# Performance work log

Measured on AMD Instinct MI355X. Metric: run time of the kernel, lower is better.

Reference implementation:

```python
import jax, jax.numpy as jnp
import numpy as np

B, T, P, F = 32, 12, 128, 128          # batch, timesteps, n_patches, nhid
NODES_PER_PATCH = 64
HORIZON = 12
N_NODES = P * NODES_PER_PATCH          # 8192


def setup_inputs() -> dict:
    key = jax.random.key(0)
    k1, k2, k3, k4 = jax.random.split(key, 4)
    x = jax.random.normal(k1, (B, T, P, F), dtype=jnp.float32)
    # per-patch Linear weights/biases, stacked: W[p] maps (nhid*T) -> (nodes_p*horizon)
    W = jax.random.normal(k2, (P, T * F, NODES_PER_PATCH * HORIZON), dtype=jnp.float32) * 0.02
    b = jax.random.normal(k3, (P, NODES_PER_PATCH * HORIZON), dtype=jnp.float32) * 0.02
    # patch -> global node indices; a permutation (each node in exactly one patch)
    patch_node_map = jax.random.permutation(k4, jnp.arange(N_NODES, dtype=jnp.int64)).reshape(P, NODES_PER_PATCH)
    return {"x": x, "W": W, "b": b, "patch_node_map": patch_node_map}


def reference(x, W, b, patch_node_map):
    # rearrange 'b t p f -> b p (t f)'
    xr = jnp.transpose(x, (0, 2, 1, 3)).reshape(x.shape[0], P, T * F)
    # grouped GEMM: one Linear per patch
    out = jnp.einsum('bpi,pio->bpo', xr, W) + b          # [B, P, nodes*H]
    out = out.reshape(x.shape[0], P * NODES_PER_PATCH, HORIZON)
    # scatter patch-local node predictions to global node positions
    out_all = jnp.zeros((x.shape[0], N_NODES, HORIZON), dtype=x.dtype)
    out_all = out_all.at[:, patch_node_map.reshape(-1), :].set(out)
    return out_all
```

## Files before the change

kernel.cpp:

```cpp
#include <hip/hip_runtime.h>


constexpr int BATCH  = 32;
constexpr int T      = 12;
constexpr int P      = 128;
constexpr int F      = 128;
constexpr int K      = T * F;
constexpr int N      = 768;
constexpr int NPP    = 64;
constexpr int H      = 12;
constexpr int NNODES = P * NPP;
constexpr int BN     = 128;
constexpr int BK     = 64;
constexpr int NT     = N / BN;

typedef __attribute__((ext_vector_type(8))) short  bf16x8;
typedef __attribute__((ext_vector_type(4))) float  f32x4;

__device__ inline short f2bf(float f) {
    unsigned u = __float_as_uint(f);
    u += 0x7fffu + ((u >> 16) & 1u);
    return (short)(u >> 16);
}

__global__ __launch_bounds__(256, 2)
void patch_readout_kernel(const float* __restrict__ x,
                          const float* __restrict__ W,
                          const float* __restrict__ bias,
                          const int*   __restrict__ map,
                          float*       __restrict__ out)
{
    __shared__ short As[2][32 * 64];

    const int p    = blockIdx.y;
    const int n0   = blockIdx.x * BN;
    const int tid  = threadIdx.x;
    const int lane = tid & 63;
    const int wv   = tid >> 6;
    const int r    = lane & 15;
    const int c    = lane >> 4;

    const int sm  = tid >> 3;
    const int skq = tid & 7;
    const float* xrow = x + (size_t)sm * T * P * F + (size_t)p * F;
    const int abyte = (sm * 128 + skq * 16) ^ ((sm & 7) << 4);

    const float* wbase = W + (size_t)p * K * N + (size_t)(8 * c) * N + (n0 + wv * 32 + r);

    f32x4 acc[2][2] = {};
    char* asbase = (char*)&As[0][0];

    int buf = 0;
    for (int k0 = 0; k0 < K; k0 += BK, buf ^= 1) {
        const int t  = k0 >> 7;
        const int fb = k0 & 127;
        const f32x4* xp = (const f32x4*)(xrow + (size_t)t * P * F + fb + skq * 8);
        f32x4 v0 = xp[0];
        f32x4 v1 = xp[1];
        bf16x8 av;
        av[0] = f2bf(v0.x); av[1] = f2bf(v0.y); av[2] = f2bf(v0.z); av[3] = f2bf(v0.w);
        av[4] = f2bf(v1.x); av[5] = f2bf(v1.y); av[6] = f2bf(v1.z); av[7] = f2bf(v1.w);
        *(bf16x8*)(asbase + buf * 4096 + abyte) = av;

        bf16x8 bfr[2][2];
        #pragma unroll
        for (int kc = 0; kc < 2; ++kc) {
            #pragma unroll
            for (int ni = 0; ni < 2; ++ni) {
                const float* wp = wbase + (size_t)(k0 + kc * 32) * N + ni * 16;
                #pragma unroll
                for (int j = 0; j < 8; ++j)
                    bfr[kc][ni][j] = f2bf(wp[(size_t)j * N]);
            }
        }

        __syncthreads();

        bf16x8 afr[2][2];
        #pragma unroll
        for (int mi = 0; mi < 2; ++mi) {
            #pragma unroll
            for (int kc = 0; kc < 2; ++kc) {
                int m    = mi * 16 + r;
                int byte = (m * 128 + kc * 64 + c * 16) ^ ((m & 7) << 4);
                afr[mi][kc] = *(const bf16x8*)(asbase + buf * 4096 + byte);
            }
        }

        #pragma unroll
        for (int mi = 0; mi < 2; ++mi)
            #pragma unroll
            for (int ni = 0; ni < 2; ++ni)
                #pragma unroll
                for (int kc = 0; kc < 2; ++kc)
                    acc[mi][ni] = __builtin_amdgcn_mfma_f32_16x16x32_bf16(
                        afr[mi][kc], bfr[kc][ni], acc[mi][ni], 0, 0, 0);
    }

    #pragma unroll
    for (int ni = 0; ni < 2; ++ni) {
        const int col = n0 + wv * 32 + ni * 16 + r;
        const int nl  = col / H;
        const int h   = col - nl * H;
        const int g   = map[p * NPP + nl];
        const float bv = bias[p * N + col];
        #pragma unroll
        for (int mi = 0; mi < 2; ++mi) {
            #pragma unroll
            for (int i = 0; i < 4; ++i) {
                const int b = mi * 16 + c * 4 + i;
                out[((size_t)b * NNODES + g) * H + h] = acc[mi][ni][i] + bv;
            }
        }
    }
}

extern "C" void kernel_launch(void* const* d_in, const int* in_sizes, int n_in,
                              void* d_out, int out_size, void* d_ws, size_t ws_size,
                              hipStream_t stream) {
    const float* x    = (const float*)d_in[0];
    const float* W    = (const float*)d_in[1];
    const float* bias = (const float*)d_in[2];
    const int*   map  = (const int*)d_in[3];
    float*       out  = (float*)d_out;

    dim3 grid(NT, P);
    dim3 block(256);
    patch_readout_kernel<<<grid, block, 0, stream>>>(x, W, bias, map, out);
}
```

Baseline: 130.3 us.

## Stage X in two large LDS halves and software-pipeline W register loads

The per-step double-buffered A tile is replaced by staging half of the activation K range (768) into LDS at once, with only two block-wide barriers mid-loop instead of one per K step. W loads are software-pipelined into two register buffers (wA/wB), so global loads for the next step are in flight during the current step's MFMAs. Launch bounds go from 2 to 3 waves per SIMD. The cost is a 48KB LDS footprint and 64 extra VGPRs of prefetch buffers, which may limit occupancy or cause spills.

```diff
diff --git a/kernel.cpp b/kernel.cpp
--- a/kernel.cpp
+++ b/kernel.cpp
@@ -1,7 +1,6 @@
 #include <hip/hip_runtime.h>
 
 
-constexpr int BATCH  = 32;
 constexpr int T      = 12;
 constexpr int P      = 128;
 constexpr int F      = 128;
@@ -11,8 +10,10 @@
 constexpr int H      = 12;
 constexpr int NNODES = P * NPP;
 constexpr int BN     = 128;
-constexpr int BK     = 64;
 constexpr int NT     = N / BN;
+constexpr int KH     = 768;
+constexpr int TPF    = T * P * F;
+constexpr int PF     = P * F;
 
 typedef __attribute__((ext_vector_type(8))) short  bf16x8;
 typedef __attribute__((ext_vector_type(4))) float  f32x4;
@@ -23,14 +24,15 @@
     return (short)(u >> 16);
 }
 
-__global__ __launch_bounds__(256, 2)
+__global__ __launch_bounds__(256, 3)
 void patch_readout_kernel(const float* __restrict__ x,
                           const float* __restrict__ W,
                           const float* __restrict__ bias,
                           const int*   __restrict__ map,
                           float*       __restrict__ out)
 {
-    __shared__ short As[2][32 * 64];
+    __shared__ short As[32 * KH];
+    char* lds = (char*)&As[0];
 
     const int p    = blockIdx.y;
     const int n0   = blockIdx.x * BN;
@@ -40,52 +42,41 @@
     const int r    = lane & 15;
     const int c    = lane >> 4;
 
-    const int sm  = tid >> 3;
-    const int skq = tid & 7;
-    const float* xrow = x + (size_t)sm * T * P * F + (size_t)p * F;
-    const int abyte = (sm * 128 + skq * 16) ^ ((sm & 7) << 4);
-
-    const float* wbase = W + (size_t)p * K * N + (size_t)(8 * c) * N + (n0 + wv * 32 + r);
+    const float* wb = W + (size_t)p * K * N + (size_t)(8 * c) * N + (n0 + wv * 32 + r);
 
     f32x4 acc[2][2] = {};
-    char* asbase = (char*)&As[0][0];
 
-    int buf = 0;
-    for (int k0 = 0; k0 < K; k0 += BK, buf ^= 1) {
-        const int t  = k0 >> 7;
-        const int fb = k0 & 127;
-        const f32x4* xp = (const f32x4*)(xrow + (size_t)t * P * F + fb + skq * 8);
-        f32x4 v0 = xp[0];
-        f32x4 v1 = xp[1];
-        bf16x8 av;
-        av[0] = f2bf(v0.x); av[1] = f2bf(v0.y); av[2] = f2bf(v0.z); av[3] = f2bf(v0.w);
-        av[4] = f2bf(v1.x); av[5] = f2bf(v1.y); av[6] = f2bf(v1.z); av[7] = f2bf(v1.w);
-        *(bf16x8*)(asbase + buf * 4096 + abyte) = av;
+    auto issueW = [&](int k0, float* wd) {
+        #pragma unroll
+        for (int kc = 0; kc < 2; ++kc)
+            #pragma unroll
+            for (int ni = 0; ni < 2; ++ni)
+                #pragma unroll
+                for (int j = 0; j < 8; ++j)
+                    wd[kc * 16 + ni * 8 + j] = wb[(size_t)(k0 + kc * 32 + j) * N + ni * 16];
+    };
 
+    auto computeStep = [&](int k0, const float* wd) {
         bf16x8 bfr[2][2];
         #pragma unroll
-        for (int kc = 0; kc < 2; ++kc) {
+        for (int kc = 0; kc < 2; ++kc)
             #pragma unroll
-            for (int ni = 0; ni < 2; ++ni) {
-                const float* wp = wbase + (size_t)(k0 + kc * 32) * N + ni * 16;
+            for (int ni = 0; ni < 2; ++ni)
                 #pragma unroll
                 for (int j = 0; j < 8; ++j)
-                    bfr[kc][ni][j] = f2bf(wp[(size_t)j * N]);
-            }
-        }
+                    bfr[kc][ni][j] = f2bf(wd[kc * 16 + ni * 8 + j]);
 
-        __syncthreads();
-
+        const int kl = (k0 >= KH) ? (k0 - KH) : k0;
+        const int kb = kl * 2;
         bf16x8 afr[2][2];
         #pragma unroll
-        for (int mi = 0; mi < 2; ++mi) {
+        for (int mi = 0; mi < 2; ++mi)
             #pragma unroll
             for (int kc = 0; kc < 2; ++kc) {
-                int m    = mi * 16 + r;
-                int byte = (m * 128 + kc * 64 + c * 16) ^ ((m & 7) << 4);
-                afr[mi][kc] = *(const bf16x8*)(asbase + buf * 4096 + byte);
+                int row  = mi * 16 + r;
+                int byte = row * (KH * 2) + ((kb + kc * 64 + c * 16) ^ ((row & 7) << 4));
+                afr[mi][kc] = *(const bf16x8*)(lds + byte);
             }
-        }
 
         #pragma unroll
         for (int mi = 0; mi < 2; ++mi)
@@ -95,6 +86,45 @@
                 for (int kc = 0; kc < 2; ++kc)
                     acc[mi][ni] = __builtin_amdgcn_mfma_f32_16x16x32_bf16(
                         afr[mi][kc], bfr[kc][ni], acc[mi][ni], 0, 0, 0);
+    };
+
+    auto stageX = [&](int half) {
+        const int row = tid >> 3;
+        const int sub = tid & 7;
+        const float* xr = x + (size_t)row * TPF + (size_t)p * F;
+        #pragma unroll
+        for (int ci = 0; ci < 12; ++ci) {
+            int k  = ci * 64 + sub * 8;
+            int kg = half * KH + k;
+            int ti = kg >> 7;
+            int f  = kg & 127;
+            const f32x4* sp = (const f32x4*)(xr + (size_t)ti * PF + f);
+            f32x4 v0 = sp[0];
+            f32x4 v1 = sp[1];
+            bf16x8 av;
+            av[0] = f2bf(v0.x); av[1] = f2bf(v0.y); av[2] = f2bf(v0.z); av[3] = f2bf(v0.w);
+            av[4] = f2bf(v1.x); av[5] = f2bf(v1.y); av[6] = f2bf(v1.z); av[7] = f2bf(v1.w);
+            *(bf16x8*)(lds + row * (KH * 2) + ((k * 2) ^ ((row & 7) << 4))) = av;
+        }
+    };
+
+    float wA[32], wB[32];
+
+    stageX(0);
+    issueW(0, wA);
+    __syncthreads();
+
+    for (int ds = 0; ds < 12; ++ds) {
+        if (ds == 6) {
+            __syncthreads();
+            stageX(1);
+            __syncthreads();
+        }
+        const int s0 = ds * 2;
+        issueW((s0 + 1) * 64, wB);
+        computeStep(s0 * 64, wA);
+        if (ds < 11) issueW((s0 + 2) * 64, wA);
+        computeStep((s0 + 1) * 64, wB);
     }
 
     #pragma unroll
```

Result: slower. 136.2 us (+4.5%).

## Load A fragments directly from global, drop LDS staging and barriers

Applied to the files above, without the earlier changes.

Each wave now loads its x fragments straight from global memory into registers instead of staging them through a double-buffered LDS tile guarded by __syncthreads. The K loop steps by 32 with partial unrolling, and the block index is remapped so consecutive blocks spread across XCDs. Occupancy is raised to three blocks per SM, and bf16 conversion now uses the HIP intrinsic. The intent is to remove barrier and LDS overhead in this W-bandwidth-bound grouped GEMM. In exchange, x is loaded redundantly by all four waves, and the higher occupancy limit may cause register pressure.

```diff
diff --git a/kernel.cpp b/kernel.cpp
--- a/kernel.cpp
+++ b/kernel.cpp
@@ -1,7 +1,7 @@
 #include <hip/hip_runtime.h>
+#include <hip/hip_bf16.h>
 
 
-constexpr int BATCH  = 32;
 constexpr int T      = 12;
 constexpr int P      = 128;
 constexpr int F      = 128;
@@ -11,90 +11,79 @@
 constexpr int H      = 12;
 constexpr int NNODES = P * NPP;
 constexpr int BN     = 128;
-constexpr int BK     = 64;
 constexpr int NT     = N / BN;
+constexpr int TPF    = T * P * F;
+constexpr int PF     = P * F;
+constexpr int NHS    = K / 32;
 
 typedef __attribute__((ext_vector_type(8))) short  bf16x8;
 typedef __attribute__((ext_vector_type(4))) float  f32x4;
 
-__device__ inline short f2bf(float f) {
-    unsigned u = __float_as_uint(f);
-    u += 0x7fffu + ((u >> 16) & 1u);
-    return (short)(u >> 16);
+union BF8 { unsigned short s[8]; bf16x8 v; };
+
+__device__ inline unsigned short f2bfu(float f) {
+    return __bfloat16_as_ushort(__float2bfloat16(f));
 }
 
-__global__ __launch_bounds__(256, 2)
+__global__ __launch_bounds__(256, 3)
 void patch_readout_kernel(const float* __restrict__ x,
                           const float* __restrict__ W,
                           const float* __restrict__ bias,
                           const int*   __restrict__ map,
                           float*       __restrict__ out)
 {
-    __shared__ short As[2][32 * 64];
+    const int bid = blockIdx.y * NT + blockIdx.x;
+    const int lgc = (bid & 7) * 96 + (bid >> 3);
+    const int p   = lgc / NT;
+    const int n0  = (lgc % NT) * BN;
 
-    const int p    = blockIdx.y;
-    const int n0   = blockIdx.x * BN;
     const int tid  = threadIdx.x;
     const int lane = tid & 63;
     const int wv   = tid >> 6;
     const int r    = lane & 15;
     const int c    = lane >> 4;
 
-    const int sm  = tid >> 3;
-    const int skq = tid & 7;
-    const float* xrow = x + (size_t)sm * T * P * F + (size_t)p * F;
-    const int abyte = (sm * 128 + skq * 16) ^ ((sm & 7) << 4);
-
-    const float* wbase = W + (size_t)p * K * N + (size_t)(8 * c) * N + (n0 + wv * 32 + r);
+    const float* wb  = W + (size_t)p * K * N + (size_t)(8 * c) * N + (n0 + wv * 32 + r);
+    const float* xb0 = x + (size_t)r * TPF        + p * F + 8 * c;
+    const float* xb1 = x + (size_t)(16 + r) * TPF + p * F + 8 * c;
 
     f32x4 acc[2][2] = {};
-    char* asbase = (char*)&As[0][0];
 
-    int buf = 0;
-    for (int k0 = 0; k0 < K; k0 += BK, buf ^= 1) {
-        const int t  = k0 >> 7;
-        const int fb = k0 & 127;
-        const f32x4* xp = (const f32x4*)(xrow + (size_t)t * P * F + fb + skq * 8);
-        f32x4 v0 = xp[0];
-        f32x4 v1 = xp[1];
-        bf16x8 av;
-        av[0] = f2bf(v0.x); av[1] = f2bf(v0.y); av[2] = f2bf(v0.z); av[3] = f2bf(v0.w);
-        av[4] = f2bf(v1.x); av[5] = f2bf(v1.y); av[6] = f2bf(v1.z); av[7] = f2bf(v1.w);
-        *(bf16x8*)(asbase + buf * 4096 + abyte) = av;
+    #pragma unroll 2
+    for (int hs = 0; hs < NHS; ++hs) {
+        const int xoff = (hs >> 2) * PF + (hs & 3) * 32;
+        const f32x4 xa0 = *(const f32x4*)(xb0 + xoff);
+        const f32x4 xa1 = *(const f32x4*)(xb0 + xoff + 4);
+        const f32x4 xa2 = *(const f32x4*)(xb1 + xoff);
+        const f32x4 xa3 = *(const f32x4*)(xb1 + xoff + 4);
 
-        bf16x8 bfr[2][2];
+        const float* wr = wb + (size_t)hs * 32 * N;
+        float wf0[8], wf1[8];
         #pragma unroll
-        for (int kc = 0; kc < 2; ++kc) {
-            #pragma unroll
-            for (int ni = 0; ni < 2; ++ni) {
-                const float* wp = wbase + (size_t)(k0 + kc * 32) * N + ni * 16;
-                #pragma unroll
-                for (int j = 0; j < 8; ++j)
-                    bfr[kc][ni][j] = f2bf(wp[(size_t)j * N]);
-            }
+        for (int j = 0; j < 8; ++j) {
+            wf0[j] = wr[j * N];
+            wf1[j] = wr[j * N + 16];
         }
 
-        __syncthreads();
-
-        bf16x8 afr[2][2];
+        BF8 ax0, ax1, bx0, bx1;
+        ax0.s[0] = f2bfu(xa0.x); ax0.s[1] = f2bfu(xa0.y);
+        ax0.s[2] = f2bfu(xa0.z); ax0.s[3] = f2bfu(xa0.w);
+        ax0.s[4] = f2bfu(xa1.x); ax0.s[5] = f2bfu(xa1.y);
+        ax0.s[6] = f2bfu(xa1.z); ax0.s[7] = f2bfu(xa1.w);
+        ax1.s[0] = f2bfu(xa2.x); ax1.s[1] = f2bfu(xa2.y);
+        ax1.s[2] = f2bfu(xa2.z); ax1.s[3] = f2bfu(xa2.w);
+        ax1.s[4] = f2bfu(xa3.x); ax1.s[5] = f2bfu(xa3.y);
+        ax1.s[6] = f2bfu(xa3.z); ax1.s[7] = f2bfu(xa3.w);
         #pragma unroll
-        for (int mi = 0; mi < 2; ++mi) {
-            #pragma unroll
-            for (int kc = 0; kc < 2; ++kc) {
-                int m    = mi * 16 + r;
-                int byte = (m * 128 + kc * 64 + c * 16) ^ ((m & 7) << 4);
-                afr[mi][kc] = *(const bf16x8*)(asbase + buf * 4096 + byte);
-            }
+        for (int j = 0; j < 8; ++j) {
+            bx0.s[j] = f2bfu(wf0[j]);
+            bx1.s[j] = f2bfu(wf1[j]);
         }
 
-        #pragma unroll
-        for (int mi = 0; mi < 2; ++mi)
-            #pragma unroll
-            for (int ni = 0; ni < 2; ++ni)
-                #pragma unroll
-                for (int kc = 0; kc < 2; ++kc)
-                    acc[mi][ni] = __builtin_amdgcn_mfma_f32_16x16x32_bf16(
-                        afr[mi][kc], bfr[kc][ni], acc[mi][ni], 0, 0, 0);
+        acc[0][0] = __builtin_amdgcn_mfma_f32_16x16x32_bf16(ax0.v, bx0.v, acc[0][0], 0, 0, 0);
+        acc[0][1] = __builtin_amdgcn_mfma_f32_16x16x32_bf16(ax0.v, bx1.v, acc[0][1], 0, 0, 0);
+        acc[1][0] = __builtin_amdgcn_mfma_f32_16x16x32_bf16(ax1.v, bx0.v, acc[1][0], 0, 0, 0);
+        acc[1][1] = __builtin_amdgcn_mfma_f32_16x16x32_bf16(ax1.v, bx1.v, acc[1][1], 0, 0, 0);
     }
 
     #pragma unroll
```

Measured after the change: 145.8 us. +11.9%, slower.

## Stage W through swizzled LDS with vectorized loads and register prefetch pipeline

Applied to the files above, without the earlier changes.

Replaces the per-lane strided scalar W loads with coalesced float4 row loads. These are converted to bf16 and transposed into a swizzled LDS tile, and MFMA B fragments are read from that tile. Adds a two-deep register prefetch so the global loads for step k+2 are in flight during compute, remaps block ids to group tiles across XCDs, and raises the occupancy hint to 3. This uses more LDS and registers per block, which may limit occupancy.

```diff
diff --git a/kernel.cpp b/kernel.cpp
--- a/kernel.cpp
+++ b/kernel.cpp
@@ -1,7 +1,7 @@
 #include <hip/hip_runtime.h>
+#include <hip/hip_bf16.h>
 
 
-constexpr int BATCH  = 32;
 constexpr int T      = 12;
 constexpr int P      = 128;
 constexpr int F      = 128;
@@ -11,90 +11,126 @@
 constexpr int H      = 12;
 constexpr int NNODES = P * NPP;
 constexpr int BN     = 128;
-constexpr int BK     = 64;
 constexpr int NT     = N / BN;
+constexpr int NSTEP  = K / 64;
+constexpr int TPF    = T * P * F;
+constexpr int PF     = P * F;
 
-typedef __attribute__((ext_vector_type(8))) short  bf16x8;
-typedef __attribute__((ext_vector_type(4))) float  f32x4;
+typedef __attribute__((ext_vector_type(8))) short        bf16x8;
+typedef __attribute__((ext_vector_type(4))) float        f32x4;
+typedef __attribute__((ext_vector_type(4))) unsigned int u32x4;
 
-__device__ inline short f2bf(float f) {
-    unsigned u = __float_as_uint(f);
-    u += 0x7fffu + ((u >> 16) & 1u);
-    return (short)(u >> 16);
+__device__ inline unsigned short f2bfu(float f) {
+    return __bfloat16_as_ushort(__float2bfloat16(f));
+}
+__device__ inline unsigned int pk2(float lo, float hi) {
+    return (unsigned int)f2bfu(lo) | ((unsigned int)f2bfu(hi) << 16);
 }
 
-__global__ __launch_bounds__(256, 2)
+__global__ __launch_bounds__(256, 3)
 void patch_readout_kernel(const float* __restrict__ x,
                           const float* __restrict__ W,
                           const float* __restrict__ bias,
                           const int*   __restrict__ map,
                           float*       __restrict__ out)
 {
-    __shared__ short As[2][32 * 64];
+    __shared__ short Wl[2][128 * 64];
+    __shared__ short Xl[2][32 * 64];
+    char* wl = (char*)&Wl[0][0];
+    char* xl = (char*)&Xl[0][0];
 
-    const int p    = blockIdx.y;
-    const int n0   = blockIdx.x * BN;
+    const int bid = blockIdx.y * NT + blockIdx.x;
+    const int lgc = (bid & 7) * 96 + (bid >> 3);
+    const int p   = lgc / NT;
+    const int n0  = (lgc % NT) * BN;
+
     const int tid  = threadIdx.x;
     const int lane = tid & 63;
     const int wv   = tid >> 6;
     const int r    = lane & 15;
     const int c    = lane >> 4;
 
-    const int sm  = tid >> 3;
-    const int skq = tid & 7;
-    const float* xrow = x + (size_t)sm * T * P * F + (size_t)p * F;
-    const int abyte = (sm * 128 + skq * 16) ^ ((sm & 7) << 4);
+    const int koct = tid >> 5;
+    const int q    = tid & 31;
+    const float* wg = W + (size_t)p * K * N + (size_t)(8 * koct) * N + (n0 + 4 * q);
 
-    const float* wbase = W + (size_t)p * K * N + (size_t)(8 * c) * N + (n0 + wv * 32 + r);
+    const int xrow = tid >> 3;
+    const int xsub = tid & 7;
+    const float* xg  = x + (size_t)xrow * TPF + p * F + xsub * 8;
+    const int    xwb = xrow * 128 + ((xsub * 16) ^ ((xrow & 7) << 4));
 
     f32x4 acc[2][2] = {};
-    char* asbase = (char*)&As[0][0];
+    f32x4 ws[8];
+    f32x4 xs[2];
 
-    int buf = 0;
-    for (int k0 = 0; k0 < K; k0 += BK, buf ^= 1) {
-        const int t  = k0 >> 7;
-        const int fb = k0 & 127;
-        const f32x4* xp = (const f32x4*)(xrow + (size_t)t * P * F + fb + skq * 8);
-        f32x4 v0 = xp[0];
-        f32x4 v1 = xp[1];
-        bf16x8 av;
-        av[0] = f2bf(v0.x); av[1] = f2bf(v0.y); av[2] = f2bf(v0.z); av[3] = f2bf(v0.w);
-        av[4] = f2bf(v1.x); av[5] = f2bf(v1.y); av[6] = f2bf(v1.z); av[7] = f2bf(v1.w);
-        *(bf16x8*)(asbase + buf * 4096 + abyte) = av;
+    auto issue = [&](int kt) {
+        const size_t kofs = (size_t)kt * 64 * N;
+        #pragma unroll
+        for (int j = 0; j < 8; ++j)
+            ws[j] = *(const f32x4*)(wg + kofs + (size_t)j * N);
+        const int xo = (kt >> 1) * PF + (kt & 1) * 64;
+        xs[0] = *(const f32x4*)(xg + xo);
+        xs[1] = *(const f32x4*)(xg + xo + 4);
+    };
 
-        bf16x8 bfr[2][2];
+    auto writeLds = [&](int d) {
+        #pragma unroll
+        for (int i = 0; i < 4; ++i) {
+            u32x4 wd;
+            wd.x = pk2(ws[0][i], ws[1][i]);
+            wd.y = pk2(ws[2][i], ws[3][i]);
+            wd.z = pk2(ws[4][i], ws[5][i]);
+            wd.w = pk2(ws[6][i], ws[7][i]);
+            const int col = 4 * q + i;
+            *(u32x4*)(wl + d * 16384 + col * 128 + ((koct * 16) ^ ((col & 7) << 4))) = wd;
+        }
+        bf16x8 xv;
+        #pragma unroll
+        for (int e = 0; e < 4; ++e) {
+            xv[e]     = (short)f2bfu(xs[0][e]);
+            xv[4 + e] = (short)f2bfu(xs[1][e]);
+        }
+        *(bf16x8*)(xl + d * 4096 + xwb) = xv;
+    };
+
+    auto compute = [&](int d) {
         #pragma unroll
         for (int kc = 0; kc < 2; ++kc) {
+            bf16x8 af[2], bfr[2];
+            #pragma unroll
+            for (int mi = 0; mi < 2; ++mi) {
+                const int row = mi * 16 + r;
+                af[mi] = *(const bf16x8*)(xl + d * 4096 + row * 128 +
+                                          ((kc * 64 + c * 16) ^ ((row & 7) << 4)));
+            }
             #pragma unroll
             for (int ni = 0; ni < 2; ++ni) {
-                const float* wp = wbase + (size_t)(k0 + kc * 32) * N + ni * 16;
+                const int col = wv * 32 + ni * 16 + r;
+                bfr[ni] = *(const bf16x8*)(wl + d * 16384 + col * 128 +
+                                           ((kc * 64 + c * 16) ^ ((col & 7) << 4)));
+            }
+            #pragma unroll
+            for (int mi = 0; mi < 2; ++mi)
                 #pragma unroll
-                for (int j = 0; j < 8; ++j)
-                    bfr[kc][ni][j] = f2bf(wp[(size_t)j * N]);
-            }
+                for (int ni = 0; ni < 2; ++ni)
+                    acc[mi][ni] = __builtin_amdgcn_mfma_f32_16x16x32_bf16(
+                        af[mi], bfr[ni], acc[mi][ni], 0, 0, 0);
         }
+    };
 
-        __syncthreads();
+    issue(0);
+    writeLds(0);
+    __syncthreads();
+    issue(1);
 
-        bf16x8 afr[2][2];
-        #pragma unroll
-        for (int mi = 0; mi < 2; ++mi) {
-            #pragma unroll
-            for (int kc = 0; kc < 2; ++kc) {
-                int m    = mi * 16 + r;
-                int byte = (m * 128 + kc * 64 + c * 16) ^ ((m & 7) << 4);
-                afr[mi][kc] = *(const bf16x8*)(asbase + buf * 4096 + byte);
-            }
+    for (int kt = 0; kt < NSTEP; ++kt) {
+        const int d = kt & 1;
+        compute(d);
+        if (kt < NSTEP - 1) {
+            writeLds(d ^ 1);
+            __syncthreads();
+            if (kt < NSTEP - 2) issue(kt + 2);
         }
-
-        #pragma unroll
-        for (int mi = 0; mi < 2; ++mi)
-            #pragma unroll
-            for (int ni = 0; ni < 2; ++ni)
-                #pragma unroll
-                for (int kc = 0; kc < 2; ++kc)
-                    acc[mi][ni] = __builtin_amdgcn_mfma_f32_16x16x32_bf16(
-                        afr[mi][kc], bfr[kc][ni], acc[mi][ni], 0, 0, 0);
     }
 
     #pragma unroll
```

Result: slower. 135.2 us (+3.7%).
